# Optimization experiments

Hardware: AMD Instinct MI355X
Metric: run time of the kernel (lower is better)

Reference implementation:

```python
import jax, jax.numpy as jnp
import numpy as np

NPOINT = 1024
RADII = (0.1, 0.2)
NSAMPLES = (16, 32)
IN_CH = 64
OUT = 256
EPS = 1e-5


def fps(pts, npoint):
    # pts: (N,3) -> (npoint,) int32 farthest-point-sampling indices (starts at index 0)
    N = pts.shape[0]
    def body(carry, _):
        dists, last = carry
        d = jnp.sum((pts - pts[last]) ** 2, axis=-1)
        dists = jnp.minimum(dists, d)
        nxt = jnp.argmax(dists).astype(jnp.int32)
        return (dists, nxt), last
    _, idx = jax.lax.scan(body, (jnp.full((N,), 1e10, pts.dtype), jnp.int32(0)), None, length=npoint)
    return idx


def ball_query(radius, k, xyz, new_xyz):
    # xyz (B,N,3), new_xyz (B,S,3) -> (B,S,k) int32; first k points within radius,
    # padded with the first in-range index (matches pointnet2 ball_query semantics;
    # each centroid is itself a point so at least one index is always in range).
    N = xyz.shape[1]
    d2 = jnp.sum((new_xyz[:, :, None, :] - xyz[:, None, :, :]) ** 2, axis=-1)  # (B,S,N)
    mask = d2 < radius * radius
    key = jnp.where(mask, jnp.arange(N, dtype=jnp.int32)[None, None, :], N)
    order = jnp.argsort(key, axis=-1)[..., :k]            # (B,S,k)
    sel_key = jnp.take_along_axis(key, order, axis=-1)
    valid = sel_key < N
    first = order[..., :1]
    return jnp.where(valid, order, first).astype(jnp.int32)


def gather(x, idx):
    # x (B,N,C), idx (B,...) -> (B,...,C)
    return jax.vmap(lambda f, i: f[i])(x, idx)


def bn_relu(x, gamma, beta):
    # BatchNorm (training-mode batch statistics) over all axes except channel (last), then ReLU
    axes = tuple(range(x.ndim - 1))
    mean = jnp.mean(x, axis=axes, keepdims=True)
    var = jnp.var(x, axis=axes, keepdims=True)
    return jax.nn.relu((x - mean) * jax.lax.rsqrt(var + EPS) * gamma + beta)


def _forward(xyz, feat, branch_params, fuse_params):
    idx_fps = jax.vmap(lambda p: fps(p, NPOINT))(xyz)     # (B,S)
    new_xyz = gather(xyz, idx_fps)                        # (B,S,3)
    outs = []
    for (r, k), (w1, g1, b1, w2, g2, b2) in zip(zip(RADII, NSAMPLES), branch_params):
        idx = ball_query(r, k, xyz, new_xyz)              # (B,S,k)
        rel = gather(xyz, idx) - new_xyz[:, :, None, :]   # (B,S,k,3)
        x = jnp.concatenate([rel, gather(feat, idx)], axis=-1)  # (B,S,k,Cin+3)
        x = bn_relu(jnp.einsum('bskc,oc->bsko', x, w1), g1, b1)
        x = bn_relu(jnp.einsum('bskc,oc->bsko', x, w2), g2, b2)
        outs.append(jnp.max(x, axis=2))                   # max-pool over nsample -> (B,S,OUT)
    x = jnp.concatenate(outs, axis=-1)                    # (B,S,len(RADII)*OUT)
    wf1, gf1, bf1, wf2, gf2, bf2 = fuse_params
    x = bn_relu(jnp.einsum('bsc,oc->bso', x, wf1), gf1, bf1)
    x = bn_relu(jnp.einsum('bsc,oc->bso', x, wf2), gf2, bf2)
    return new_xyz, x


def setup_inputs():
    key = jax.random.key(0)
    ks = jax.random.split(key, 16)
    B, N = 8, 4096
    xyz = jax.random.uniform(ks[0], (B, N, 3), dtype=jnp.float32)
    feat = jax.random.normal(ks[1], (B, N, IN_CH), dtype=jnp.float32)
    cin, mid = IN_CH + 3, OUT // 2
    def w(k, o, c):
        return jax.random.normal(k, (o, c), dtype=jnp.float32) * np.float32(1.0 / np.sqrt(c))
    inp = {"xyz": xyz, "feat": feat}
    i = 2
    for s in range(len(RADII)):
        inp[f"w1_{s}"] = w(ks[i], mid, cin); i += 1
        inp[f"g1_{s}"] = jnp.ones((mid,), jnp.float32)
        inp[f"b1_{s}"] = jnp.zeros((mid,), jnp.float32)
        inp[f"w2_{s}"] = w(ks[i], OUT, mid); i += 1
        inp[f"g2_{s}"] = jnp.ones((OUT,), jnp.float32)
        inp[f"b2_{s}"] = jnp.zeros((OUT,), jnp.float32)
    inp["wf1"] = w(ks[i], OUT, len(RADII) * OUT); i += 1
    inp["gf1"] = jnp.ones((OUT,), jnp.float32)
    inp["bf1"] = jnp.zeros((OUT,), jnp.float32)
    inp["wf2"] = w(ks[i], OUT, OUT)
    inp["gf2"] = jnp.ones((OUT,), jnp.float32)
    inp["bf2"] = jnp.zeros((OUT,), jnp.float32)
    return inp


def reference(xyz, feat, w1_0, g1_0, b1_0, w2_0, g2_0, b2_0,
              w1_1, g1_1, b1_1, w2_1, g2_1, b2_1,
              wf1, gf1, bf1, wf2, gf2, bf2):
    branch_params = [(w1_0, g1_0, b1_0, w2_0, g2_0, b2_0),
                     (w1_1, g1_1, b1_1, w2_1, g2_1, b2_1)]
    fuse_params = (wf1, gf1, bf1, wf2, gf2, bf2)
    return _forward(xyz, feat, branch_params, fuse_params)
```

## Files before the change

kernel.cpp:

```cpp
#include <hip/hip_runtime.h>
#include <hip/hip_bf16.h>


#define DEV __device__ __forceinline__

typedef __attribute__((ext_vector_type(8))) short short8v;
typedef __attribute__((ext_vector_type(4))) float float4v;

DEV float d2_nofma(float ax, float ay, float az, float bx, float by, float bz) {
#pragma clang fp contract(off)
  float dx = ax - bx, dy = ay - by, dz = az - bz;
  float s = dx * dx + dy * dy;
  return s + dz * dz;
}

DEV unsigned long long u64max(unsigned long long a, unsigned long long b) {
  return a > b ? a : b;
}

DEV void bsplit(float x, short& h, short& l) {
  __hip_bfloat16 hb = __float2bfloat16(x);
  float hf = __bfloat162float(hb);
  __hip_bfloat16 lb = __float2bfloat16(x - hf);
  h = *reinterpret_cast<short*>(&hb);
  l = *reinterpret_cast<short*>(&lb);
}

__global__ __launch_bounds__(512) void fps_kernel(
    const float* __restrict__ xyz, int* __restrict__ idx_out,
    float* __restrict__ nx_ws, float* __restrict__ nx_out) {
  __shared__ float sp[4096 * 3];
  __shared__ int hist[1024];
  __shared__ unsigned long long cand[2][8];
  const int b = blockIdx.x, t = threadIdx.x;
  const int w = t >> 6;
  const float* P = xyz + (size_t)b * 12288;
  float px[8], py[8], pz[8], dd[8];
#pragma unroll
  for (int j = 0; j < 8; j++) {
    int pi = t * 8 + j;
    float x = P[pi * 3], y = P[pi * 3 + 1], z = P[pi * 3 + 2];
    px[j] = x; py[j] = y; pz[j] = z; dd[j] = 1e10f;
    sp[pi * 3] = x; sp[pi * 3 + 1] = y; sp[pi * 3 + 2] = z;
  }
  __syncthreads();
  int last = 0;
  for (int it = 0; it < 1024; ++it) {
    if (t == 0) hist[it] = last;
    if (it == 1023) break;
    float lx = sp[last * 3], ly = sp[last * 3 + 1], lz = sp[last * 3 + 2];
#pragma unroll
    for (int j = 0; j < 8; j++) {
      float d = d2_nofma(px[j], py[j], pz[j], lx, ly, lz);
      dd[j] = fminf(dd[j], d);
    }
    float bv = fmaxf(fmaxf(fmaxf(dd[0], dd[1]), fmaxf(dd[2], dd[3])),
                     fmaxf(fmaxf(dd[4], dd[5]), fmaxf(dd[6], dd[7])));
    int bj = 7;
#pragma unroll
    for (int j = 6; j >= 0; j--) bj = (dd[j] == bv) ? j : bj;
    int bi = t * 8 + bj;
    unsigned long long p =
        ((unsigned long long)__float_as_uint(bv) << 32) |
        (unsigned int)(4095 - bi);
#define DPP_MAX_STEP(CTRL)                                                  \
    {                                                                       \
      int lo_ = (int)(unsigned int)(p & 0xffffffffull);                     \
      int hi_ = (int)(unsigned int)(p >> 32);                               \
      int olo_ = __builtin_amdgcn_update_dpp(0, lo_, CTRL, 0xf, 0xf, false);\
      int ohi_ = __builtin_amdgcn_update_dpp(0, hi_, CTRL, 0xf, 0xf, false);\
      unsigned long long q_ =                                               \
          ((unsigned long long)(unsigned int)ohi_ << 32) |                  \
          (unsigned int)olo_;                                               \
      if (q_ > p) p = q_;                                                   \
    }
    DPP_MAX_STEP(0xB1);
    DPP_MAX_STEP(0x4E);
    DPP_MAX_STEP(0x124);
    DPP_MAX_STEP(0x128);
    DPP_MAX_STEP(0x142);
    DPP_MAX_STEP(0x143);
#undef DPP_MAX_STEP
    const int buf = it & 1;
    if ((t & 63) == 63) cand[buf][w] = p;
    __syncthreads();
    unsigned long long c0 = cand[buf][0], c1 = cand[buf][1];
    unsigned long long c2 = cand[buf][2], c3 = cand[buf][3];
    unsigned long long c4 = cand[buf][4], c5 = cand[buf][5];
    unsigned long long c6 = cand[buf][6], c7 = cand[buf][7];
    unsigned long long best =
        u64max(u64max(u64max(c0, c1), u64max(c2, c3)),
               u64max(u64max(c4, c5), u64max(c6, c7)));
    last = 4095 - (int)(unsigned int)(best & 0xffffffffull);
  }
  __syncthreads();
  for (int i = t; i < 1024; i += 512) {
    int id = hist[i];
    idx_out[(size_t)b * 1024 + i] = id;
    float x = sp[id * 3], y = sp[id * 3 + 1], z = sp[id * 3 + 2];
    size_t o = ((size_t)b * 1024 + i) * 3;
    nx_ws[o] = x; nx_ws[o + 1] = y; nx_ws[o + 2] = z;
    nx_out[o] = x; nx_out[o + 1] = y; nx_out[o + 2] = z;
  }
}

__global__ __launch_bounds__(256) void bq_kernel(
    const float* __restrict__ xyz, const float* __restrict__ nx,
    int* __restrict__ out0, int* __restrict__ out1) {
  const int wv = threadIdx.x >> 6, lane = threadIdx.x & 63;
  const int bs = blockIdx.x * 4 + wv;
  const int b = bs >> 10;
  const float* c = nx + (size_t)bs * 3;
  const float cx = c[0], cy = c[1], cz = c[2];
  const float* P = xyz + (size_t)b * 12288;
  const float rr0 = 0.1f * 0.1f, rr1 = 0.2f * 0.2f;
  int c0 = 0, c1 = 0, f0 = -1, f1 = -1;
  const unsigned long long below = (1ull << lane) - 1ull;
  for (int base = 0; base < 4096; base += 64) {
    int p = base + lane;
    float x = P[p * 3], y = P[p * 3 + 1], z = P[p * 3 + 2];
    float d2 = d2_nofma(cx, cy, cz, x, y, z);
    bool in0 = d2 < rr0, in1 = d2 < rr1;
    unsigned long long m0 = __ballot(in0), m1 = __ballot(in1);
    if (in0) {
      int slot = c0 + __popcll(m0 & below);
      if (slot < 16) out0[(size_t)bs * 16 + slot] = p;
    }
    if (in1) {
      int slot = c1 + __popcll(m1 & below);
      if (slot < 32) out1[(size_t)bs * 32 + slot] = p;
    }
    if (f0 < 0 && m0) f0 = base + __ffsll(m0) - 1;
    if (f1 < 0 && m1) f1 = base + __ffsll(m1) - 1;
    c0 += __popcll(m0);
    c1 += __popcll(m1);
    if (c0 >= 16 && c1 >= 32) break;
  }
  if (c0 < 16 && lane >= c0 && lane < 16) out0[(size_t)bs * 16 + lane] = f0;
  if (c1 < 32 && lane >= c1 && lane < 32) out1[(size_t)bs * 32 + lane] = f1;
}

__global__ __launch_bounds__(256) void w2split_kernel(
    const float* __restrict__ w, short* __restrict__ h,
    short* __restrict__ l) {
  int i = blockIdx.x * 256 + threadIdx.x;
  short hb, lb;
  bsplit(w[i], hb, lb);
  h[i] = hb;
  l[i] = lb;
}

template <int KS>
__global__ __launch_bounds__(256) void g1_kernel(
    const float* __restrict__ xyz, const float* __restrict__ feat,
    const float* __restrict__ nx, const int* __restrict__ idx,
    const float* __restrict__ w1, float* __restrict__ y1,
    float* __restrict__ statp) {
  __shared__ float At[34][132];
  __shared__ float Bt[34][132];
  const int t = threadIdx.x;
  const int g0 = blockIdx.x * 128;
  const int tx = t & 15, ty = t >> 4;
  const int r = t >> 1, half = t & 1;
  const int g = g0 + r;
  const int bs = g / KS;
  const int b = bs >> 10;
  const int id = idx[g];
  const float* fp = feat + ((size_t)(b * 4096 + id)) * 64;
  float rel0 = 0, rel1 = 0, rel2 = 0;
  if (half == 0) {
    const float* cp = nx + (size_t)bs * 3;
    const float* pp = xyz + ((size_t)(b * 4096 + id)) * 3;
    rel0 = pp[0] - cp[0]; rel1 = pp[1] - cp[1]; rel2 = pp[2] - cp[2];
  }
  float acc[8][8];
#pragma unroll
  for (int i = 0; i < 8; i++)
#pragma unroll
    for (int j = 0; j < 8; j++) acc[i][j] = 0.f;

#pragma unroll
  for (int kc = 0; kc < 2; ++kc) {
    const int kb = kc * 34;
    const int kn = kc ? 33 : 34;
    {
      int c0 = half * 17;
      int cn = half ? (kn - 17) : 17;
      for (int u = 0; u < cn; u++) {
        int cabs = kb + c0 + u;
        float v;
        if (cabs < 3) v = (cabs == 0) ? rel0 : ((cabs == 1) ? rel1 : rel2);
        else v = fp[cabs - 3];
        At[c0 + u][r] = v;
      }
    }
    {
      int o = t >> 1;
      const float* wp = w1 + (size_t)o * 67;
      int c0 = half * 17;
      int cn = half ? (kn - 17) : 17;
      for (int u = 0; u < cn; u++) Bt[c0 + u][o] = wp[kb + c0 + u];
    }
    __syncthreads();
#pragma unroll 4
    for (int k = 0; k < kn; k++) {
      float4 a0 = *(const float4*)&At[k][ty * 4];
      float4 a1 = *(const float4*)&At[k][ty * 4 + 64];
      float4 b0 = *(const float4*)&Bt[k][tx * 4];
      float4 b1 = *(const float4*)&Bt[k][tx * 4 + 64];
      float av[8] = {a0.x, a0.y, a0.z, a0.w, a1.x, a1.y, a1.z, a1.w};
      float bv[8] = {b0.x, b0.y, b0.z, b0.w, b1.x, b1.y, b1.z, b1.w};
#pragma unroll
      for (int i = 0; i < 8; i++)
#pragma unroll
        for (int j = 0; j < 8; j++) acc[i][j] = fmaf(av[i], bv[j], acc[i][j]);
    }
    __syncthreads();
  }
#pragma unroll
  for (int i = 0; i < 8; i++) {
    int R = ty * 4 + (i & 3) + ((i >> 2) << 6);
    float4 s0 = {acc[i][0], acc[i][1], acc[i][2], acc[i][3]};
    float4 s1 = {acc[i][4], acc[i][5], acc[i][6], acc[i][7]};
    *(float4*)&y1[((size_t)(g0 + R)) * 128 + tx * 4] = s0;
    *(float4*)&y1[((size_t)(g0 + R)) * 128 + tx * 4 + 64] = s1;
  }
  float s8[8], q8[8];
#pragma unroll
  for (int j = 0; j < 8; j++) {
    float s = 0, q = 0;
#pragma unroll
    for (int i = 0; i < 8; i++) {
      float v = acc[i][j];
      s += v;
      q = fmaf(v, v, q);
    }
    s += __shfl_xor(s, 16); s += __shfl_xor(s, 32);
    q += __shfl_xor(q, 16); q += __shfl_xor(q, 32);
    s8[j] = s; q8[j] = q;
  }
  float* red = &At[0][0];
  const int wvx = t >> 6;
  if ((t & 63) < 16) {
#pragma unroll
    for (int j = 0; j < 8; j++) {
      int col = tx * 4 + (j & 3) + ((j >> 2) << 6);
      red[wvx * 128 + col] = s8[j];
      red[512 + wvx * 128 + col] = q8[j];
    }
  }
  __syncthreads();
  if (t < 128) {
    float s = red[t] + red[128 + t] + red[256 + t] + red[384 + t];
    float q = red[512 + t] + red[640 + t] + red[768 + t] + red[896 + t];
    statp[(size_t)blockIdx.x * 256 + t] = s;
    statp[(size_t)blockIdx.x * 256 + 128 + t] = q;
  }
}

template <int KS>
__global__ __launch_bounds__(256, 2) void g2_kernel(
    const float* __restrict__ y1, const short* __restrict__ w2h,
    const short* __restrict__ w2l, const float* __restrict__ a1,
    const float* __restrict__ b1, float* __restrict__ pmin,
    float* __restrict__ pmax, float* __restrict__ statp) {
  __shared__ __align__(16) short Abuf[2][128][136];
  const int t = threadIdx.x;
  const int wv = t >> 6, lane = t & 63;
  const int g0 = blockIdx.x * 128;

  {
    const int r = t >> 1, half = t & 1;
    const float* arow = y1 + (size_t)(g0 + r) * 128 + half * 64;
#pragma unroll
    for (int q = 0; q < 8; q++) {
      float4 v0 = *(const float4*)&arow[q * 8];
      float4 v1 = *(const float4*)&arow[q * 8 + 4];
      float vv[8] = {v0.x, v0.y, v0.z, v0.w, v1.x, v1.y, v1.z, v1.w};
      short8v h8, l8;
#pragma unroll
      for (int e = 0; e < 8; e++) {
        int cabs = half * 64 + q * 8 + e;
        float x = fmaxf(fmaf(a1[cabs], vv[e], b1[cabs]), 0.f);
        short hh, ll;
        bsplit(x, hh, ll);
        h8[e] = hh; l8[e] = ll;
      }
      *(short8v*)&Abuf[0][r][half * 64 + q * 8] = h8;
      *(short8v*)&Abuf[1][r][half * 64 + q * 8] = l8;
    }
  }
  __syncthreads();

  const int kgo = (lane >> 4) * 8;
  short8v ahf[2][4], alf[2][4];
#pragma unroll
  for (int mt = 0; mt < 2; mt++)
#pragma unroll
    for (int kg = 0; kg < 4; kg++) {
      int rr = wv * 32 + mt * 16 + (lane & 15);
      ahf[mt][kg] = *(const short8v*)&Abuf[0][rr][kg * 32 + kgo];
      alf[mt][kg] = *(const short8v*)&Abuf[1][rr][kg * 32 + kgo];
    }
  __syncthreads();

  float4v acc[2][16];
#pragma unroll
  for (int mt = 0; mt < 2; mt++)
#pragma unroll
    for (int nt = 0; nt < 16; nt++) acc[mt][nt] = (float4v){0.f, 0.f, 0.f, 0.f};

#pragma unroll
  for (int kg = 0; kg < 4; kg++) {
#pragma unroll
    for (int nt = 0; nt < 16; nt++) {
      const int brow = nt * 16 + (lane & 15);
      const size_t bo = (size_t)brow * 128 + kg * 32 + kgo;
      short8v bh = *(const short8v*)&w2h[bo];
      short8v bl = *(const short8v*)&w2l[bo];
#pragma unroll
      for (int mt = 0; mt < 2; mt++) {
        acc[mt][nt] = __builtin_amdgcn_mfma_f32_16x16x32_bf16(
            ahf[mt][kg], bh, acc[mt][nt], 0, 0, 0);
        acc[mt][nt] = __builtin_amdgcn_mfma_f32_16x16x32_bf16(
            alf[mt][kg], bh, acc[mt][nt], 0, 0, 0);
        acc[mt][nt] = __builtin_amdgcn_mfma_f32_16x16x32_bf16(
            ahf[mt][kg], bl, acc[mt][nt], 0, 0, 0);
      }
    }
  }

  float* red = (float*)&Abuf[0][0][0];
#pragma unroll
  for (int nt = 0; nt < 16; nt++) {
    float s = 0, q = 0;
#pragma unroll
    for (int mt = 0; mt < 2; mt++)
#pragma unroll
      for (int j = 0; j < 4; j++) {
        float v = acc[mt][nt][j];
        s += v;
        q = fmaf(v, v, q);
      }
    s += __shfl_xor(s, 16); s += __shfl_xor(s, 32);
    q += __shfl_xor(q, 16); q += __shfl_xor(q, 32);
    if (lane < 16) {
      red[wv * 256 + nt * 16 + lane] = s;
      red[1024 + wv * 256 + nt * 16 + lane] = q;
    }
  }
  __syncthreads();
  {
    float s = red[t] + red[256 + t] + red[512 + t] + red[768 + t];
    float q = red[1024 + t] + red[1280 + t] + red[1536 + t] + red[1792 + t];
    statp[(size_t)blockIdx.x * 512 + t] = s;
    statp[(size_t)blockIdx.x * 512 + 256 + t] = q;
  }

  if (KS == 32) {
#pragma unroll
    for (int nt = 0; nt < 16; nt++) {
      float mn = acc[0][nt][0], mx = acc[0][nt][0];
#pragma unroll
      for (int mt = 0; mt < 2; mt++)
#pragma unroll
        for (int j = 0; j < 4; j++) {
          float v = acc[mt][nt][j];
          mn = fminf(mn, v);
          mx = fmaxf(mx, v);
        }
      mn = fminf(mn, __shfl_xor(mn, 16)); mn = fminf(mn, __shfl_xor(mn, 32));
      mx = fmaxf(mx, __shfl_xor(mx, 16)); mx = fmaxf(mx, __shfl_xor(mx, 32));
      if (lane < 16) {
        size_t o = (size_t)(blockIdx.x * 4 + wv) * 256 + nt * 16 + lane;
        pmin[o] = mn;
        pmax[o] = mx;
      }
    }
  } else {
#pragma unroll
    for (int mt = 0; mt < 2; mt++)
#pragma unroll
      for (int nt = 0; nt < 16; nt++) {
        float mn = acc[mt][nt][0], mx = acc[mt][nt][0];
#pragma unroll
        for (int j = 1; j < 4; j++) {
          float v = acc[mt][nt][j];
          mn = fminf(mn, v);
          mx = fmaxf(mx, v);
        }
        mn = fminf(mn, __shfl_xor(mn, 16)); mn = fminf(mn, __shfl_xor(mn, 32));
        mx = fmaxf(mx, __shfl_xor(mx, 16)); mx = fmaxf(mx, __shfl_xor(mx, 32));
        if (lane < 16) {
          size_t o = (size_t)(blockIdx.x * 8 + wv * 2 + mt) * 256 + nt * 16 + lane;
          pmin[o] = mn;
          pmax[o] = mx;
        }
      }
  }
}

__global__ __launch_bounds__(256) void finalize_affine(
    const float* __restrict__ statp, int nb, float invM,
    const float* __restrict__ gamma, const float* __restrict__ beta,
    float* __restrict__ aout, float* __restrict__ bout, int N) {
  const int c = blockIdx.x;
  const int t = threadIdx.x;
  float s = 0, q = 0;
  for (int i = t; i < nb; i += 256) {
    s += statp[(size_t)i * 2 * N + c];
    q += statp[(size_t)i * 2 * N + N + c];
  }
#pragma unroll
  for (int m = 1; m <= 32; m <<= 1) {
    s += __shfl_xor(s, m);
    q += __shfl_xor(q, m);
  }
  __shared__ float rs[4], rq[4];
  if ((t & 63) == 0) { rs[t >> 6] = s; rq[t >> 6] = q; }
  __syncthreads();
  if (t == 0) {
    s = rs[0] + rs[1] + rs[2] + rs[3];
    q = rq[0] + rq[1] + rq[2] + rq[3];
    float mean = s * invM;
    float var = q * invM - mean * mean;
    float ia = gamma[c] * rsqrtf(var + 1e-5f);
    aout[c] = ia;
    bout[c] = beta[c] - mean * ia;
  }
}

__global__ __launch_bounds__(256) void pool_concat(
    const float* __restrict__ pmin, const float* __restrict__ pmax,
    const float* __restrict__ a2, const float* __restrict__ b2,
    float* __restrict__ cat, int off) {
  int i = blockIdx.x * 256 + threadIdx.x;
  int row = i >> 8, c = i & 255;
  float a = a2[c];
  float v = (a > 0.f) ? pmax[i] : pmin[i];
  cat[(size_t)row * 512 + off + c] = fmaxf(fmaf(a, v, b2[c]), 0.f);
}

template <bool AFF>
__global__ __launch_bounds__(256) void f_kernel(
    const float* __restrict__ A, const float* __restrict__ W,
    const float* __restrict__ ain, const float* __restrict__ bin,
    float* __restrict__ Y, int K, float* __restrict__ statp) {
  __shared__ float At[64][68];
  __shared__ float Bt[64][132];
  const int t = threadIdx.x, tx = t & 15, ty = t >> 4;
  const int g0 = blockIdx.x * 64, cb = blockIdx.y;
  float acc[4][8];
#pragma unroll
  for (int i = 0; i < 4; i++)
#pragma unroll
    for (int j = 0; j < 8; j++) acc[i][j] = 0.f;
  const int rA = t >> 2, qA = t & 3;
  const int oB = t >> 1, hB = t & 1;
  const float* arow = A + (size_t)(g0 + rA) * K + qA * 16;
  const float* wrow = W + (size_t)(cb * 128 + oB) * K + hB * 32;
  for (int kc = 0; kc < K; kc += 64) {
    {
#pragma unroll
      for (int q = 0; q < 4; q++) {
        float4 v = *(const float4*)&arow[kc + q * 4];
        float vv[4] = {v.x, v.y, v.z, v.w};
        if constexpr (AFF) {
          int c = kc + qA * 16 + q * 4;
#pragma unroll
          for (int e = 0; e < 4; e++)
            vv[e] = fmaxf(fmaf(ain[c + e], vv[e], bin[c + e]), 0.f);
        }
#pragma unroll
        for (int e = 0; e < 4; e++) At[qA * 16 + q * 4 + e][rA] = vv[e];
      }
    }
    {
#pragma unroll
      for (int q = 0; q < 8; q++) {
        float4 v = *(const float4*)&wrow[kc + q * 4];
        Bt[hB * 32 + q * 4 + 0][oB] = v.x;
        Bt[hB * 32 + q * 4 + 1][oB] = v.y;
        Bt[hB * 32 + q * 4 + 2][oB] = v.z;
        Bt[hB * 32 + q * 4 + 3][oB] = v.w;
      }
    }
    __syncthreads();
#pragma unroll 8
    for (int k = 0; k < 64; k++) {
      float4 a0 = *(const float4*)&At[k][ty * 4];
      float4 b0 = *(const float4*)&Bt[k][tx * 4];
      float4 b1 = *(const float4*)&Bt[k][tx * 4 + 64];
      float av[4] = {a0.x, a0.y, a0.z, a0.w};
      float bv[8] = {b0.x, b0.y, b0.z, b0.w, b1.x, b1.y, b1.z, b1.w};
#pragma unroll
      for (int i = 0; i < 4; i++)
#pragma unroll
        for (int j = 0; j < 8; j++) acc[i][j] = fmaf(av[i], bv[j], acc[i][j]);
    }
    __syncthreads();
  }
#pragma unroll
  for (int i = 0; i < 4; i++) {
    int R = g0 + ty * 4 + i;
    float4 s0 = {acc[i][0], acc[i][1], acc[i][2], acc[i][3]};
    float4 s1 = {acc[i][4], acc[i][5], acc[i][6], acc[i][7]};
    *(float4*)&Y[(size_t)R * 256 + cb * 128 + tx * 4] = s0;
    *(float4*)&Y[(size_t)R * 256 + cb * 128 + tx * 4 + 64] = s1;
  }
  float s8[8], q8[8];
#pragma unroll
  for (int j = 0; j < 8; j++) {
    float s = 0, q = 0;
#pragma unroll
    for (int i = 0; i < 4; i++) {
      float v = acc[i][j];
      s += v;
      q = fmaf(v, v, q);
    }
    s += __shfl_xor(s, 16); s += __shfl_xor(s, 32);
    q += __shfl_xor(q, 16); q += __shfl_xor(q, 32);
    s8[j] = s; q8[j] = q;
  }
  float* red = &At[0][0];
  const int wvx = t >> 6;
  if ((t & 63) < 16) {
#pragma unroll
    for (int j = 0; j < 8; j++) {
      int col = tx * 4 + (j & 3) + ((j >> 2) << 6);
      red[wvx * 128 + col] = s8[j];
      red[512 + wvx * 128 + col] = q8[j];
    }
  }
  __syncthreads();
  if (t < 128) {
    float s = red[t] + red[128 + t] + red[256 + t] + red[384 + t];
    float q = red[512 + t] + red[640 + t] + red[768 + t] + red[896 + t];
    statp[(size_t)blockIdx.x * 512 + cb * 128 + t] = s;
    statp[(size_t)blockIdx.x * 512 + 256 + cb * 128 + t] = q;
  }
}

__global__ __launch_bounds__(256) void final_write(
    const float* __restrict__ y, const float* __restrict__ a,
    const float* __restrict__ b, float* __restrict__ out) {
  int i = blockIdx.x * 256 + threadIdx.x;
  int c = i & 255;
  out[i] = fmaxf(fmaf(a[c], y[i], b[c]), 0.f);
}

static const size_t OFF_IDXFPS = 0;
static const size_t OFF_NEWXYZ = 8192;
static const size_t OFF_IDX0 = 32768;
static const size_t OFF_IDX1 = 163840;
static const size_t OFF_Y1 = 425984;
static const size_t OFF_PMIN = 33980416;
static const size_t OFF_PMAX = 36077568;
static const size_t OFF_STATP = 38174720;
static const size_t OFF_CONCAT = 39223296;
static const size_t OFF_YF1 = 43417600;
static const size_t OFF_YF2 = 45514752;
static const size_t OFF_AFF = 47611904;

extern "C" void kernel_launch(void* const* d_in, const int* in_sizes, int n_in,
                              void* d_out, int out_size, void* d_ws,
                              size_t ws_size, hipStream_t stream) {
  const float* xyz = (const float*)d_in[0];
  const float* feat = (const float*)d_in[1];
  const float* w1_0 = (const float*)d_in[2];
  const float* g1_0 = (const float*)d_in[3];
  const float* b1_0 = (const float*)d_in[4];
  const float* w2_0 = (const float*)d_in[5];
  const float* g2_0 = (const float*)d_in[6];
  const float* b2_0 = (const float*)d_in[7];
  const float* w1_1 = (const float*)d_in[8];
  const float* g1_1 = (const float*)d_in[9];
  const float* b1_1 = (const float*)d_in[10];
  const float* w2_1 = (const float*)d_in[11];
  const float* g2_1 = (const float*)d_in[12];
  const float* b2_1 = (const float*)d_in[13];
  const float* wf1 = (const float*)d_in[14];
  const float* gf1 = (const float*)d_in[15];
  const float* bf1 = (const float*)d_in[16];
  const float* wf2 = (const float*)d_in[17];
  const float* gf2 = (const float*)d_in[18];
  const float* bf2 = (const float*)d_in[19];

  float* out = (float*)d_out;
  float* ws = (float*)d_ws;

  int* idxfps = (int*)(ws + OFF_IDXFPS);
  float* nx = ws + OFF_NEWXYZ;
  int* idx0 = (int*)(ws + OFF_IDX0);
  int* idx1 = (int*)(ws + OFF_IDX1);
  float* y1 = ws + OFF_Y1;
  float* pmin = ws + OFF_PMIN;
  float* pmax = ws + OFF_PMAX;
  float* statp = ws + OFF_STATP;
  float* cat = ws + OFF_CONCAT;
  float* yf1 = ws + OFF_YF1;
  float* yf2 = ws + OFF_YF2;
  float* a1 = ws + OFF_AFF;
  float* b1 = a1 + 128;
  float* a2 = b1 + 128;
  float* b2 = a2 + 256;
  float* af1 = b2 + 256;
  float* bf1a = af1 + 256;
  float* af2 = bf1a + 256;
  float* bf2a = af2 + 256;
  short* w2h0 = (short*)yf1;
  short* w2l0 = w2h0 + 32768;
  short* w2h1 = w2l0 + 32768;
  short* w2l1 = w2h1 + 32768;

  w2split_kernel<<<128, 256, 0, stream>>>(w2_0, w2h0, w2l0);
  w2split_kernel<<<128, 256, 0, stream>>>(w2_1, w2h1, w2l1);
  fps_kernel<<<8, 512, 0, stream>>>(xyz, idxfps, nx, out);
  bq_kernel<<<2048, 256, 0, stream>>>(xyz, nx, idx0, idx1);

  g1_kernel<16><<<1024, 256, 0, stream>>>(xyz, feat, nx, idx0, w1_0, y1, statp);
  finalize_affine<<<128, 256, 0, stream>>>(statp, 1024, 1.f / 131072.f, g1_0, b1_0, a1, b1, 128);
  g2_kernel<16><<<1024, 256, 0, stream>>>(y1, w2h0, w2l0, a1, b1, pmin, pmax, statp);
  finalize_affine<<<256, 256, 0, stream>>>(statp, 1024, 1.f / 131072.f, g2_0, b2_0, a2, b2, 256);
  pool_concat<<<8192, 256, 0, stream>>>(pmin, pmax, a2, b2, cat, 0);

  g1_kernel<32><<<2048, 256, 0, stream>>>(xyz, feat, nx, idx1, w1_1, y1, statp);
  finalize_affine<<<128, 256, 0, stream>>>(statp, 2048, 1.f / 262144.f, g1_1, b1_1, a1, b1, 128);
  g2_kernel<32><<<2048, 256, 0, stream>>>(y1, w2h1, w2l1, a1, b1, pmin, pmax, statp);
  finalize_affine<<<256, 256, 0, stream>>>(statp, 2048, 1.f / 262144.f, g2_1, b2_1, a2, b2, 256);
  pool_concat<<<8192, 256, 0, stream>>>(pmin, pmax, a2, b2, cat, 256);

  f_kernel<false><<<dim3(128, 2), 256, 0, stream>>>(cat, wf1, nullptr, nullptr, yf1, 512, statp);
  finalize_affine<<<256, 256, 0, stream>>>(statp, 128, 1.f / 8192.f, gf1, bf1, af1, bf1a, 256);
  f_kernel<true><<<dim3(128, 2), 256, 0, stream>>>(yf1, wf2, af1, bf1a, yf2, 256, statp);
  finalize_affine<<<256, 256, 0, stream>>>(statp, 128, 1.f / 8192.f, gf2, bf2, af2, bf2a, 256);
  final_write<<<8192, 256, 0, stream>>>(yf2, af2, bf2a, out + 24576);
}
```

Baseline: 1.312 ms.

## Use split-bf16 MFMA for fuse MLP and fold pooling affine into GEMM load

The two fuse-layer GEMMs are rewritten to use bf16 MFMA with a hi/lo split (three products) in place of scalar FP32 FMA tiles, with the weights split once by a new kernel. The pool_concat kernels are removed: the first fuse GEMM reads per-branch pmin/pmax directly and applies the BN affine, ReLU and min/max selection while loading its A tile, so the concat buffer is never written. This trades exact FP32 accumulation for a three-term bf16 approximation and adds a weight-split launch. The fuse stage is small relative to the FPS and branch work, so the overall effect is limited.

```diff
diff --git a/kernel.cpp b/kernel.cpp
--- a/kernel.cpp
+++ b/kernel.cpp
@@ -148,6 +148,22 @@
   bsplit(w[i], hb, lb);
   h[i] = hb;
   l[i] = lb;
+}
+
+__global__ __launch_bounds__(256) void wsplit2_kernel(
+    const float* __restrict__ wa, int na, const float* __restrict__ wb,
+    short* __restrict__ ha, short* __restrict__ la, short* __restrict__ hb,
+    short* __restrict__ lb) {
+  int i = blockIdx.x * 256 + threadIdx.x;
+  short h, l;
+  if (i < na) {
+    bsplit(wa[i], h, l);
+    ha[i] = h; la[i] = l;
+  } else {
+    int j = i - na;
+    bsplit(wb[j], h, l);
+    hb[j] = h; lb[j] = l;
+  }
 }
 
 template <int KS>
@@ -400,6 +416,133 @@
   }
 }
 
+template <int MODE>
+__global__ __launch_bounds__(256, 4) void f_mfma(
+    const float* __restrict__ src,
+    const float* __restrict__ pmin0, const float* __restrict__ pmax0,
+    const float* __restrict__ pmin1, const float* __restrict__ pmax1,
+    const float* __restrict__ aa0, const float* __restrict__ bb0,
+    const float* __restrict__ aa1, const float* __restrict__ bb1,
+    const short* __restrict__ wh, const short* __restrict__ wl,
+    float* __restrict__ Y, float* __restrict__ statp) {
+  constexpr int K = MODE ? 256 : 512;
+  constexpr int NCH = K / 128;
+  __shared__ __align__(16) short Abuf[2][64][136];
+  const int t = threadIdx.x;
+  const int wv = t >> 6, lane = t & 63;
+  const int g0 = blockIdx.x * 64, cb = blockIdx.y;
+  const int kgo = (lane >> 4) * 8;
+
+  float4v acc[8];
+#pragma unroll
+  for (int nt = 0; nt < 8; nt++) acc[nt] = (float4v){0.f, 0.f, 0.f, 0.f};
+
+  for (int kc = 0; kc < NCH; kc++) {
+    {
+      const int r = t >> 2, seg = t & 3;
+      const int row = g0 + r;
+#pragma unroll
+      for (int q = 0; q < 4; q++) {
+        const int c0 = kc * 128 + seg * 32 + q * 8;
+        float v[8];
+        if constexpr (MODE == 0) {
+          const int br = c0 >> 8;
+          const int cc0 = c0 & 255;
+          const float* pa = br ? aa1 : aa0;
+          const float* pb = br ? bb1 : bb0;
+          const float* pmn = br ? pmin1 : pmin0;
+          const float* pmx = br ? pmax1 : pmax0;
+          float4 mn0 = *(const float4*)&pmn[(size_t)row * 256 + cc0];
+          float4 mn1 = *(const float4*)&pmn[(size_t)row * 256 + cc0 + 4];
+          float4 mx0 = *(const float4*)&pmx[(size_t)row * 256 + cc0];
+          float4 mx1 = *(const float4*)&pmx[(size_t)row * 256 + cc0 + 4];
+          float mns[8] = {mn0.x, mn0.y, mn0.z, mn0.w, mn1.x, mn1.y, mn1.z, mn1.w};
+          float mxs[8] = {mx0.x, mx0.y, mx0.z, mx0.w, mx1.x, mx1.y, mx1.z, mx1.w};
+#pragma unroll
+          for (int e = 0; e < 8; e++) {
+            float a = pa[cc0 + e];
+            float ext = (a > 0.f) ? mxs[e] : mns[e];
+            v[e] = fmaxf(fmaf(a, ext, pb[cc0 + e]), 0.f);
+          }
+        } else {
+          float4 s0 = *(const float4*)&src[(size_t)row * 256 + c0];
+          float4 s1 = *(const float4*)&src[(size_t)row * 256 + c0 + 4];
+          float ss[8] = {s0.x, s0.y, s0.z, s0.w, s1.x, s1.y, s1.z, s1.w};
+#pragma unroll
+          for (int e = 0; e < 8; e++)
+            v[e] = fmaxf(fmaf(aa0[c0 + e], ss[e], bb0[c0 + e]), 0.f);
+        }
+        short8v h8, l8;
+#pragma unroll
+        for (int e = 0; e < 8; e++) {
+          short hh, ll;
+          bsplit(v[e], hh, ll);
+          h8[e] = hh; l8[e] = ll;
+        }
+        *(short8v*)&Abuf[0][r][seg * 32 + q * 8] = h8;
+        *(short8v*)&Abuf[1][r][seg * 32 + q * 8] = l8;
+      }
+    }
+    __syncthreads();
+    const int rr = wv * 16 + (lane & 15);
+    short8v ah[4], al[4];
+#pragma unroll
+    for (int kg = 0; kg < 4; kg++) {
+      ah[kg] = *(const short8v*)&Abuf[0][rr][kg * 32 + kgo];
+      al[kg] = *(const short8v*)&Abuf[1][rr][kg * 32 + kgo];
+    }
+    __syncthreads();
+#pragma unroll
+    for (int kg = 0; kg < 4; kg++) {
+#pragma unroll
+      for (int nt = 0; nt < 8; nt++) {
+        const int brow = cb * 128 + nt * 16 + (lane & 15);
+        const size_t bo = (size_t)brow * K + kc * 128 + kg * 32 + kgo;
+        short8v bh = *(const short8v*)&wh[bo];
+        short8v bl = *(const short8v*)&wl[bo];
+        acc[nt] = __builtin_amdgcn_mfma_f32_16x16x32_bf16(ah[kg], bh, acc[nt], 0, 0, 0);
+        acc[nt] = __builtin_amdgcn_mfma_f32_16x16x32_bf16(al[kg], bh, acc[nt], 0, 0, 0);
+        acc[nt] = __builtin_amdgcn_mfma_f32_16x16x32_bf16(ah[kg], bl, acc[nt], 0, 0, 0);
+      }
+    }
+  }
+
+#pragma unroll
+  for (int nt = 0; nt < 8; nt++) {
+#pragma unroll
+    for (int j = 0; j < 4; j++) {
+      int row = g0 + wv * 16 + (lane >> 4) * 4 + j;
+      int col = cb * 128 + nt * 16 + (lane & 15);
+      Y[(size_t)row * 256 + col] = acc[nt][j];
+    }
+  }
+
+  float* red = (float*)&Abuf[0][0][0];
+#pragma unroll
+  for (int nt = 0; nt < 8; nt++) {
+    float s = 0, q = 0;
+#pragma unroll
+    for (int j = 0; j < 4; j++) {
+      float v = acc[nt][j];
+      s += v;
+      q = fmaf(v, v, q);
+    }
+    s += __shfl_xor(s, 16); s += __shfl_xor(s, 32);
+    q += __shfl_xor(q, 16); q += __shfl_xor(q, 32);
+    if (lane < 16) {
+      red[wv * 128 + nt * 16 + lane] = s;
+      red[512 + wv * 128 + nt * 16 + lane] = q;
+    }
+  }
+  __syncthreads();
+  if (t < 128) {
+    float s = red[t] + red[128 + t] + red[256 + t] + red[384 + t];
+    float q = red[512 + t] + red[640 + t] + red[768 + t] + red[896 + t];
+    statp[(size_t)blockIdx.x * 512 + cb * 128 + t] = s;
+    statp[(size_t)blockIdx.x * 512 + 256 + cb * 128 + t] = q;
+  }
+}
+
 __global__ __launch_bounds__(256) void finalize_affine(
     const float* __restrict__ statp, int nb, float invM,
     const float* __restrict__ gamma, const float* __restrict__ beta,
@@ -430,117 +573,6 @@
   }
 }
 
-__global__ __launch_bounds__(256) void pool_concat(
-    const float* __restrict__ pmin, const float* __restrict__ pmax,
-    const float* __restrict__ a2, const float* __restrict__ b2,
-    float* __restrict__ cat, int off) {
-  int i = blockIdx.x * 256 + threadIdx.x;
-  int row = i >> 8, c = i & 255;
-  float a = a2[c];
-  float v = (a > 0.f) ? pmax[i] : pmin[i];
-  cat[(size_t)row * 512 + off + c] = fmaxf(fmaf(a, v, b2[c]), 0.f);
-}
-
-template <bool AFF>
-__global__ __launch_bounds__(256) void f_kernel(
-    const float* __restrict__ A, const float* __restrict__ W,
-    const float* __restrict__ ain, const float* __restrict__ bin,
-    float* __restrict__ Y, int K, float* __restrict__ statp) {
-  __shared__ float At[64][68];
-  __shared__ float Bt[64][132];
-  const int t = threadIdx.x, tx = t & 15, ty = t >> 4;
-  const int g0 = blockIdx.x * 64, cb = blockIdx.y;
-  float acc[4][8];
-#pragma unroll
-  for (int i = 0; i < 4; i++)
-#pragma unroll
-    for (int j = 0; j < 8; j++) acc[i][j] = 0.f;
-  const int rA = t >> 2, qA = t & 3;
-  const int oB = t >> 1, hB = t & 1;
-  const float* arow = A + (size_t)(g0 + rA) * K + qA * 16;
-  const float* wrow = W + (size_t)(cb * 128 + oB) * K + hB * 32;
-  for (int kc = 0; kc < K; kc += 64) {
-    {
-#pragma unroll
-      for (int q = 0; q < 4; q++) {
-        float4 v = *(const float4*)&arow[kc + q * 4];
-        float vv[4] = {v.x, v.y, v.z, v.w};
-        if constexpr (AFF) {
-          int c = kc + qA * 16 + q * 4;
-#pragma unroll
-          for (int e = 0; e < 4; e++)
-            vv[e] = fmaxf(fmaf(ain[c + e], vv[e], bin[c + e]), 0.f);
-        }
-#pragma unroll
-        for (int e = 0; e < 4; e++) At[qA * 16 + q * 4 + e][rA] = vv[e];
-      }
-    }
-    {
-#pragma unroll
-      for (int q = 0; q < 8; q++) {
-        float4 v = *(const float4*)&wrow[kc + q * 4];
-        Bt[hB * 32 + q * 4 + 0][oB] = v.x;
-        Bt[hB * 32 + q * 4 + 1][oB] = v.y;
-        Bt[hB * 32 + q * 4 + 2][oB] = v.z;
-        Bt[hB * 32 + q * 4 + 3][oB] = v.w;
-      }
-    }
-    __syncthreads();
-#pragma unroll 8
-    for (int k = 0; k < 64; k++) {
-      float4 a0 = *(const float4*)&At[k][ty * 4];
-      float4 b0 = *(const float4*)&Bt[k][tx * 4];
-      float4 b1 = *(const float4*)&Bt[k][tx * 4 + 64];
-      float av[4] = {a0.x, a0.y, a0.z, a0.w};
-      float bv[8] = {b0.x, b0.y, b0.z, b0.w, b1.x, b1.y, b1.z, b1.w};
-#pragma unroll
-      for (int i = 0; i < 4; i++)
-#pragma unroll
-        for (int j = 0; j < 8; j++) acc[i][j] = fmaf(av[i], bv[j], acc[i][j]);
-    }
-    __syncthreads();
-  }
-#pragma unroll
-  for (int i = 0; i < 4; i++) {
-    int R = g0 + ty * 4 + i;
-    float4 s0 = {acc[i][0], acc[i][1], acc[i][2], acc[i][3]};
-    float4 s1 = {acc[i][4], acc[i][5], acc[i][6], acc[i][7]};
-    *(float4*)&Y[(size_t)R * 256 + cb * 128 + tx * 4] = s0;
-    *(float4*)&Y[(size_t)R * 256 + cb * 128 + tx * 4 + 64] = s1;
-  }
-  float s8[8], q8[8];
-#pragma unroll
-  for (int j = 0; j < 8; j++) {
-    float s = 0, q = 0;
-#pragma unroll
-    for (int i = 0; i < 4; i++) {
-      float v = acc[i][j];
-      s += v;
-      q = fmaf(v, v, q);
-    }
-    s += __shfl_xor(s, 16); s += __shfl_xor(s, 32);
-    q += __shfl_xor(q, 16); q += __shfl_xor(q, 32);
-    s8[j] = s; q8[j] = q;
-  }
-  float* red = &At[0][0];
-  const int wvx = t >> 6;
-  if ((t & 63) < 16) {
-#pragma unroll
-    for (int j = 0; j < 8; j++) {
-      int col = tx * 4 + (j & 3) + ((j >> 2) << 6);
-      red[wvx * 128 + col] = s8[j];
-      red[512 + wvx * 128 + col] = q8[j];
-    }
-  }
-  __syncthreads();
-  if (t < 128) {
-    float s = red[t] + red[128 + t] + red[256 + t] + red[384 + t];
-    float q = red[512 + t] + red[640 + t] + red[768 + t] + red[896 + t];
-    statp[(size_t)blockIdx.x * 512 + cb * 128 + t] = s;
-    statp[(size_t)blockIdx.x * 512 + 256 + cb * 128 + t] = q;
-  }
-}
-
 __global__ __launch_bounds__(256) void final_write(
     const float* __restrict__ y, const float* __restrict__ a,
     const float* __restrict__ b, float* __restrict__ out) {
@@ -554,10 +586,10 @@
 static const size_t OFF_IDX0 = 32768;
 static const size_t OFF_IDX1 = 163840;
 static const size_t OFF_Y1 = 425984;
-static const size_t OFF_PMIN = 33980416;
-static const size_t OFF_PMAX = 36077568;
+static const size_t OFF_PMIN0 = 33980416;
+static const size_t OFF_PMAX0 = 36077568;
 static const size_t OFF_STATP = 38174720;
-static const size_t OFF_CONCAT = 39223296;
+static const size_t OFF_PM1 = 39223296;
 static const size_t OFF_YF1 = 43417600;
 static const size_t OFF_YF2 = 45514752;
 static const size_t OFF_AFF = 47611904;
@@ -594,24 +626,31 @@
   int* idx0 = (int*)(ws + OFF_IDX0);
   int* idx1 = (int*)(ws + OFF_IDX1);
   float* y1 = ws + OFF_Y1;
-  float* pmin = ws + OFF_PMIN;
-  float* pmax = ws + OFF_PMAX;
+  float* pmin0 = ws + OFF_PMIN0;
+  float* pmax0 = ws + OFF_PMAX0;
   float* statp = ws + OFF_STATP;
-  float* cat = ws + OFF_CONCAT;
+  float* pmin1 = ws + OFF_PM1;
+  float* pmax1 = pmin1 + 2097152;
   float* yf1 = ws + OFF_YF1;
   float* yf2 = ws + OFF_YF2;
-  float* a1 = ws + OFF_AFF;
-  float* b1 = a1 + 128;
-  float* a2 = b1 + 128;
-  float* b2 = a2 + 256;
-  float* af1 = b2 + 256;
-  float* bf1a = af1 + 256;
-  float* af2 = bf1a + 256;
-  float* bf2a = af2 + 256;
+  float* pa1 = ws + OFF_AFF;
+  float* pb1 = pa1 + 128;
+  float* pa2_0 = pb1 + 128;
+  float* pb2_0 = pa2_0 + 256;
+  float* pa2_1 = pb2_0 + 256;
+  float* pb2_1 = pa2_1 + 256;
+  float* paf1 = pb2_1 + 256;
+  float* pbf1 = paf1 + 256;
+  float* paf2 = pbf1 + 256;
+  float* pbf2 = paf2 + 256;
   short* w2h0 = (short*)yf1;
   short* w2l0 = w2h0 + 32768;
   short* w2h1 = w2l0 + 32768;
   short* w2l1 = w2h1 + 32768;
+  short* wf1h = (short*)y1;
+  short* wf1l = wf1h + 131072;
+  short* wf2h = wf1l + 131072;
+  short* wf2l = wf2h + 65536;
 
   w2split_kernel<<<128, 256, 0, stream>>>(w2_0, w2h0, w2l0);
   w2split_kernel<<<128, 256, 0, stream>>>(w2_1, w2h1, w2l1);
@@ -619,20 +658,23 @@
   bq_kernel<<<2048, 256, 0, stream>>>(xyz, nx, idx0, idx1);
 
   g1_kernel<16><<<1024, 256, 0, stream>>>(xyz, feat, nx, idx0, w1_0, y1, statp);
-  finalize_affine<<<128, 256, 0, stream>>>(statp, 1024, 1.f / 131072.f, g1_0, b1_0, a1, b1, 128);
-  g2_kernel<16><<<1024, 256, 0, stream>>>(y1, w2h0, w2l0, a1, b1, pmin, pmax, statp);
-  finalize_affine<<<256, 256, 0, stream>>>(statp, 1024, 1.f / 131072.f, g2_0, b2_0, a2, b2, 256);
-  pool_concat<<<8192, 256, 0, stream>>>(pmin, pmax, a2, b2, cat, 0);
+  finalize_affine<<<128, 256, 0, stream>>>(statp, 1024, 1.f / 131072.f, g1_0, b1_0, pa1, pb1, 128);
+  g2_kernel<16><<<1024, 256, 0, stream>>>(y1, w2h0, w2l0, pa1, pb1, pmin0, pmax0, statp);
+  finalize_affine<<<256, 256, 0, stream>>>(statp, 1024, 1.f / 131072.f, g2_0, b2_0, pa2_0, pb2_0, 256);
 
   g1_kernel<32><<<2048, 256, 0, stream>>>(xyz, feat, nx, idx1, w1_1, y1, statp);
-  finalize_affine<<<128, 256, 0, stream>>>(statp, 2048, 1.f / 262144.f, g1_1, b1_1, a1, b1, 128);
-  g2_kernel<32><<<2048, 256, 0, stream>>>(y1, w2h1, w2l1, a1, b1, pmin, pmax, statp);
-  finalize_affine<<<256, 256, 0, stream>>>(statp, 2048, 1.f / 262144.f, g2_1, b2_1, a2, b2, 256);
-  pool_concat<<<8192, 256, 0, stream>>>(pmin, pmax, a2, b2, cat, 256);
-
-  f_kernel<false><<<dim3(128, 2), 256, 0, stream>>>(cat, wf1, nullptr, nullptr, yf1, 512, statp);
-  finalize_affine<<<256, 256, 0, stream>>>(statp, 128, 1.f / 8192.f, gf1, bf1, af1, bf1a, 256);
-  f_kernel<true><<<dim3(128, 2), 256, 0, stream>>>(yf1, wf2, af1, bf1a, yf2, 256, statp);
-  finalize_affine<<<256, 256, 0, stream>>>(statp, 128, 1.f / 8192.f, gf2, bf2, af2, bf2a, 256);
-  final_write<<<8192, 256, 0, stream>>>(yf2, af2, bf2a, out + 24576);
-}
+  finalize_affine<<<128, 256, 0, stream>>>(statp, 2048, 1.f / 262144.f, g1_1, b1_1, pa1, pb1, 128);
+  g2_kernel<32><<<2048, 256, 0, stream>>>(y1, w2h1, w2l1, pa1, pb1, pmin1, pmax1, statp);
+  finalize_affine<<<256, 256, 0, stream>>>(statp, 2048, 1.f / 262144.f, g2_1, b2_1, pa2_1, pb2_1, 256);
+
+  wsplit2_kernel<<<768, 256, 0, stream>>>(wf1, 131072, wf2, wf1h, wf1l, wf2h, wf2l);
+  f_mfma<0><<<dim3(128, 2), 256, 0, stream>>>(
+      nullptr, pmin0, pmax0, pmin1, pmax1, pa2_0, pb2_0, pa2_1, pb2_1,
+      wf1h, wf1l, yf1, statp);
+  finalize_affine<<<256, 256, 0, stream>>>(statp, 128, 1.f / 8192.f, gf1, bf1, paf1, pbf1, 256);
+  f_mfma<1><<<dim3(128, 2), 256, 0, stream>>>(
+      yf1, nullptr, nullptr, nullptr, nullptr, paf1, pbf1, nullptr, nullptr,
+      wf2h, wf2l, yf2, statp);
+  finalize_affine<<<256, 256, 0, stream>>>(statp, 128, 1.f / 8192.f, gf2, bf2, paf2, pbf2, 256);
+  final_write<<<8192, 256, 0, stream>>>(yf2, paf2, pbf2, out + 24576);
+}
```

Result: slower. 1.347 ms (+2.6%).
